# Performance work log

Measured on AMD Instinct MI355X. Metric: run time of the kernel, lower is better.

Reference implementation:

```python
import jax, jax.numpy as jnp
import numpy as np

EPS = 1e-5

def rms_norm(x):
    # SimpleRMSNorm (no learned weight), as used inside BitLinear158
    return x * jax.lax.rsqrt(jnp.mean(x * x, axis=-1, keepdims=True) + EPS)

def act_quant(x):
    # int8 absmax quantization per last-dim row, with straight-through estimator
    scale = 127.0 / jnp.clip(jnp.max(jnp.abs(x), axis=-1, keepdims=True), 1e-5)
    q = jnp.clip(jnp.round(x * scale), -128.0, 127.0) / scale
    return x + jax.lax.stop_gradient(q - x)

def weight_quant(w):
    # ternary {-1,0,1} absmean quantization, with straight-through estimator
    scale = 1.0 / jnp.clip(jnp.mean(jnp.abs(w)), 1e-5)
    q = jnp.clip(jnp.round(w * scale), -1.0, 1.0) / scale
    return w + jax.lax.stop_gradient(q - w)

def bitlinear158(x, w, b):
    xq = act_quant(rms_norm(x))          # [b,s,d_in]
    wq = weight_quant(w)                 # [d_out,d_in]
    return jnp.einsum('bsd,od->bso', xq, wq) + b

def layer_norm(x, g, b):
    mu = jnp.mean(x, axis=-1, keepdims=True)
    var = jnp.mean((x - mu) ** 2, axis=-1, keepdims=True)
    return (x - mu) * jax.lax.rsqrt(var + EPS) * g + b

def setup_inputs() -> dict:
    key = jax.random.key(0)
    ks = jax.random.split(key, 3)
    d, inner = 2048, 8192
    x = jax.random.normal(ks[0], (4, 2048, d), dtype=jnp.float32)
    w1 = jax.random.normal(ks[1], (inner, d), dtype=jnp.float32) * 0.02
    b1 = jnp.zeros((inner,), jnp.float32)
    ln_g = jnp.ones((inner,), jnp.float32)
    ln_b = jnp.zeros((inner,), jnp.float32)
    w2 = jax.random.normal(ks[2], (d, inner), dtype=jnp.float32) * 0.02
    b2 = jnp.zeros((d,), jnp.float32)
    return {"x": x, "w1": w1, "b1": b1, "ln_g": ln_g, "ln_b": ln_b, "w2": w2, "b2": b2}

def reference(x, w1, b1, ln_g, ln_b, w2, b2):
    h = jax.nn.silu(bitlinear158(x, w1, b1))        # project_in: BitLinear158 + SiLU
    h = jax.nn.gelu(h, approximate=False)            # nn.GELU (exact erf form)
    h = layer_norm(h, ln_g, ln_b)                    # nn.LayerNorm(inner_dim)
    return bitlinear158(h, w2, b2)                   # BitLinear158 out projection
```

## Files before the change

### kernel.cpp

```cpp
#include <hip/hip_runtime.h>
#include <hip/hip_bf16.h>
#include <math.h>

typedef __bf16 bf16_t;
typedef __bf16 bf16x4 __attribute__((ext_vector_type(4)));
typedef int i32x4 __attribute__((ext_vector_type(4)));

#define AS1 __attribute__((address_space(1)))
#define AS3 __attribute__((address_space(3)))

__device__ __forceinline__ void gl_lds16(const char* g, char* l) {
  __builtin_amdgcn_global_load_lds((const AS1 void*)g, (AS3 void*)l, 16, 0, 0);
}

__device__ __forceinline__ unsigned pack4i(float a, float b, float c, float d) {
  return ((unsigned)(unsigned char)(int)a) | ((unsigned)(unsigned char)(int)b << 8) |
         ((unsigned)(unsigned char)(int)c << 16) | ((unsigned)(unsigned char)(int)d << 24);
}

__device__ __forceinline__ float block_sum_f(float v) {
  __shared__ float sb[4];
  #pragma unroll
  for (int o = 32; o; o >>= 1) v += __shfl_xor(v, o);
  if ((threadIdx.x & 63) == 0) sb[threadIdx.x >> 6] = v;
  __syncthreads();
  v = sb[0] + sb[1] + sb[2] + sb[3];
  __syncthreads();
  return v;
}
__device__ __forceinline__ float block_max_f(float v) {
  __shared__ float sm[4];
  #pragma unroll
  for (int o = 32; o; o >>= 1) v = fmaxf(v, __shfl_xor(v, o));
  if ((threadIdx.x & 63) == 0) sm[threadIdx.x >> 6] = v;
  __syncthreads();
  v = fmaxf(fmaxf(sm[0], sm[1]), fmaxf(sm[2], sm[3]));
  __syncthreads();
  return v;
}

__global__ __launch_bounds__(256) void wabs_partial(const float* __restrict__ w, int n4,
                                                    double* __restrict__ part) {
  const float4* w4 = (const float4*)w;
  double s = 0.0;
  const int stride = gridDim.x * blockDim.x;
  for (int i = blockIdx.x * blockDim.x + threadIdx.x; i < n4; i += stride) {
    float4 v = w4[i];
    s += (double)fabsf(v.x) + (double)fabsf(v.y) + (double)fabsf(v.z) + (double)fabsf(v.w);
  }
  #pragma unroll
  for (int o = 32; o; o >>= 1) s += __shfl_xor(s, o);
  __shared__ double sd[4];
  if ((threadIdx.x & 63) == 0) sd[threadIdx.x >> 6] = s;
  __syncthreads();
  if (threadIdx.x == 0) part[blockIdx.x] = sd[0] + sd[1] + sd[2] + sd[3];
}

__global__ __launch_bounds__(256) void wabs_final(const double* __restrict__ part, int np,
                                                  double n, float* __restrict__ fwout) {
  double s = 0.0;
  for (int i = threadIdx.x; i < np; i += blockDim.x) s += part[i];
  #pragma unroll
  for (int o = 32; o; o >>= 1) s += __shfl_xor(s, o);
  __shared__ double sd[4];
  if ((threadIdx.x & 63) == 0) sd[threadIdx.x >> 6] = s;
  __syncthreads();
  if (threadIdx.x == 0) {
    double mean = (sd[0] + sd[1] + sd[2] + sd[3]) / n;
    fwout[0] = (float)fmax(mean, 1e-5);
  }
}

__global__ __launch_bounds__(256) void quant_w(const float* __restrict__ w,
                                               const float* __restrict__ fw,
                                               char* __restrict__ wq, int n4) {
  int i = blockIdx.x * blockDim.x + threadIdx.x;
  if (i >= n4) return;
  const float s = 1.0f / fw[0];
  float4 v = ((const float4*)w)[i];
  ((unsigned*)wq)[i] = pack4i(fminf(fmaxf(rintf(v.x * s), -1.f), 1.f),
                              fminf(fmaxf(rintf(v.y * s), -1.f), 1.f),
                              fminf(fmaxf(rintf(v.z * s), -1.f), 1.f),
                              fminf(fmaxf(rintf(v.w * s), -1.f), 1.f));
}

__global__ __launch_bounds__(256) void rms_quant_x(const float* __restrict__ x,
                                                   char* __restrict__ xq,
                                                   float* __restrict__ fx, int K) {
  const int row = blockIdx.x, t = threadIdx.x;
  const size_t base = (size_t)row * K;
  float v[8];
  float ss = 0.f;
  #pragma unroll
  for (int j = 0; j < 2; j++) {
    float4 lv = *(const float4*)(x + base + j * 1024 + t * 4);
    v[j*4+0] = lv.x; v[j*4+1] = lv.y; v[j*4+2] = lv.z; v[j*4+3] = lv.w;
  }
  #pragma unroll
  for (int i = 0; i < 8; i++) ss += v[i] * v[i];
  ss = block_sum_f(ss);
  const float r = 1.0f / sqrtf(ss / (float)K + 1e-5f);
  float amax = 0.f;
  #pragma unroll
  for (int i = 0; i < 8; i++) { v[i] *= r; amax = fmaxf(amax, fabsf(v[i])); }
  amax = block_max_f(amax);
  amax = fmaxf(amax, 1e-5f);
  const float scale = 127.0f / amax;
  #pragma unroll
  for (int j = 0; j < 2; j++) {
    float q[4];
    #pragma unroll
    for (int e = 0; e < 4; e++)
      q[e] = fminf(fmaxf(rintf(v[j*4+e] * scale), -128.f), 127.f);
    *(unsigned*)(xq + base + j * 1024 + t * 4) = pack4i(q[0], q[1], q[2], q[3]);
  }
  if (t == 0) fx[row] = amax / 127.0f;
}

__global__ __launch_bounds__(256) void ln_rms_quant(const bf16_t* __restrict__ h,
                                                    char* __restrict__ hq,
                                                    const float* __restrict__ g,
                                                    const float* __restrict__ bb,
                                                    float* __restrict__ fh, int N) {
  const int row = blockIdx.x, t = threadIdx.x;
  const size_t base = (size_t)row * N;
  float v[32];
  float s = 0.f, ss = 0.f;
  #pragma unroll
  for (int j = 0; j < 8; j++) {
    const int col = j * 1024 + t * 4;
    bf16x4 q = *(const bf16x4*)(h + base + col);
    v[j*4+0] = (float)q[0]; v[j*4+1] = (float)q[1];
    v[j*4+2] = (float)q[2]; v[j*4+3] = (float)q[3];
  }
  #pragma unroll
  for (int i = 0; i < 32; i++) { s += v[i]; ss += v[i] * v[i]; }
  s = block_sum_f(s);
  ss = block_sum_f(ss);
  const float mu = s / (float)N;
  const float var = ss / (float)N - mu * mu;
  const float rstd = 1.0f / sqrtf(var + 1e-5f);
  float ss2 = 0.f;
  #pragma unroll
  for (int j = 0; j < 8; j++) {
    const int col = j * 1024 + t * 4;
    float4 gv = *(const float4*)(g + col);
    float4 bv = *(const float4*)(bb + col);
    float y0 = (v[j*4+0] - mu) * rstd * gv.x + bv.x;
    float y1 = (v[j*4+1] - mu) * rstd * gv.y + bv.y;
    float y2 = (v[j*4+2] - mu) * rstd * gv.z + bv.z;
    float y3 = (v[j*4+3] - mu) * rstd * gv.w + bv.w;
    v[j*4+0] = y0; v[j*4+1] = y1; v[j*4+2] = y2; v[j*4+3] = y3;
    ss2 += y0*y0 + y1*y1 + y2*y2 + y3*y3;
  }
  ss2 = block_sum_f(ss2);
  const float r2 = 1.0f / sqrtf(ss2 / (float)N + 1e-5f);
  float amax = 0.f;
  #pragma unroll
  for (int i = 0; i < 32; i++) { v[i] *= r2; amax = fmaxf(amax, fabsf(v[i])); }
  amax = block_max_f(amax);
  amax = fmaxf(amax, 1e-5f);
  const float scale = 127.0f / amax;
  #pragma unroll
  for (int j = 0; j < 8; j++) {
    const int col = j * 1024 + t * 4;
    float q[4];
    #pragma unroll
    for (int e = 0; e < 4; e++)
      q[e] = fminf(fmaxf(rintf(v[j*4+e] * scale), -128.f), 127.f);
    *(unsigned*)(hq + base + col) = pack4i(q[0], q[1], q[2], q[3]);
  }
  if (t == 0) fh[row] = amax / 127.0f;
}

template<int EPI, bool STORE_BF16>
__global__ __launch_bounds__(512, 2) void gemm256(const char* __restrict__ A,
                                                  const char* __restrict__ B,
                                                  const float* __restrict__ rowf,
                                                  const float* __restrict__ wf,
                                                  const float* __restrict__ bias,
                                                  float* __restrict__ Cf,
                                                  bf16_t* __restrict__ Cb,
                                                  int M, int N, int K) {
  __shared__ char smem[131072];

  const int ntile = N >> 8;
  const int cpx = gridDim.x >> 3;
  const int bid = blockIdx.x;
  const int xcd = bid & 7, local = bid >> 3;
  int wg;
  const int mrows = cpx / ntile;
  if (mrows * ntile == cpx && mrows > 0) {
    const int bm_l = local % mrows, bn_i = local / mrows;
    wg = (xcd * mrows + bm_l) * ntile + bn_i;
  } else {
    wg = xcd * cpx + local;
  }
  const int bm = wg / ntile, bn = wg % ntile;
  const int tm = bm << 8, tn = bn << 8;

  const int tid = threadIdx.x;
  const int w = tid >> 6, lane = tid & 63;
  const int wm = w >> 2, wn = w & 3;
  const int ln15 = lane & 15;

  const int srow = lane >> 3;
  const int scol = ((lane & 7) ^ srow) << 4;
  const size_t KS = (size_t)K;
  const char* pAst = A + (size_t)(tm + w * 16 + srow) * KS + scol;
  const char* pBst = B + (size_t)(tn + w * 16 + srow) * KS + scol;
  const size_t hiO = (size_t)128 * KS;
  const size_t r8 = (size_t)8 * KS;
  const int dW = w * 2048;

  int foffk[2];
  #pragma unroll
  for (int kk = 0; kk < 2; kk++)
    foffk[kk] = ln15 * 128 + ((((kk << 2) + (lane >> 4)) ^ (ln15 & 7)) << 4);

  i32x4 acc[8][4] = {};
  const int NT = K >> 7;

#define SB __builtin_amdgcn_sched_barrier(0)
#define BAR { SB; __builtin_amdgcn_s_barrier(); SB; }
#define ST_A(bb, hh, kt) { const char* p = pAst + ((hh) ? hiO : 0) + (size_t)(kt) * 128; \
    char* dst = smem + (bb) * 32768 + (hh) * 16384 + dW;                                 \
    gl_lds16(p, dst); gl_lds16(p + r8, dst + 1024); }
#define ST_B(bb, hh, kt) { const char* p = pBst + ((hh) ? hiO : 0) + (size_t)(kt) * 128; \
    char* dst = smem + 65536 + (bb) * 32768 + (hh) * 16384 + dW;                         \
    gl_lds16(p, dst); gl_lds16(p + r8, dst + 1024); }
#define MM(AF, BF, MB, NB)                                                   \
  _Pragma("unroll") for (int kk = 0; kk < 2; kk++)                           \
    _Pragma("unroll") for (int m4 = 0; m4 < 4; m4++)                         \
      _Pragma("unroll") for (int n2 = 0; n2 < 2; n2++)                       \
        acc[(MB)+m4][(NB)+n2] = __builtin_amdgcn_mfma_i32_16x16x64_i8(       \
            AF[m4][kk], BF[n2][kk], acc[(MB)+m4][(NB)+n2], 0, 0, 0);
#define VM(n) asm volatile("s_waitcnt vmcnt(" #n ")" ::: "memory")

  ST_A(0, 0, 0); ST_B(0, 0, 0); ST_B(0, 1, 0); ST_A(0, 1, 0);

  for (int t = 0; t < NT; ++t) {
    const int b = t & 1, nb = b ^ 1;
    const char* sA = smem + b * 32768;
    const char* sB = smem + 65536 + b * 32768;
    i32x4 afL[4][2], afH[4][2], bL[2][2], bH[2][2];
    if (t + 1 < NT) { ST_A(nb, 0, t + 1); ST_B(nb, 0, t + 1); VM(8); }
    else            { VM(4); }
    BAR;
    #pragma unroll
    for (int m4 = 0; m4 < 4; m4++)
      #pragma unroll
      for (int kk = 0; kk < 2; kk++)
        afL[m4][kk] = *(const i32x4*)(sA + (wm * 4 + m4) * 2048 + foffk[kk]);
    #pragma unroll
    for (int n2 = 0; n2 < 2; n2++)
      #pragma unroll
      for (int kk = 0; kk < 2; kk++)
        bL[n2][kk] = *(const i32x4*)(sB + (wn * 2 + n2) * 2048 + foffk[kk]);
    __builtin_amdgcn_s_setprio(1);
    MM(afL, bL, 0, 0);
    __builtin_amdgcn_s_setprio(0);
    if (t + 1 < NT) { ST_B(nb, 1, t + 1); VM(8); }
    else            { VM(2); }
    BAR;
    #pragma unroll
    for (int n2 = 0; n2 < 2; n2++)
      #pragma unroll
      for (int kk = 0; kk < 2; kk++)
        bH[n2][kk] = *(const i32x4*)(sB + 16384 + (wn * 2 + n2) * 2048 + foffk[kk]);
    __builtin_amdgcn_s_setprio(1);
    MM(afL, bH, 0, 2);
    __builtin_amdgcn_s_setprio(0);
    if (t + 1 < NT) { ST_A(nb, 1, t + 1); VM(8); }
    else            { VM(0); }
    BAR;
    #pragma unroll
    for (int m4 = 0; m4 < 4; m4++)
      #pragma unroll
      for (int kk = 0; kk < 2; kk++)
        afH[m4][kk] = *(const i32x4*)(sA + 16384 + (wm * 4 + m4) * 2048 + foffk[kk]);
    __builtin_amdgcn_s_setprio(1);
    MM(afH, bH, 4, 2);
    __builtin_amdgcn_s_setprio(0);
    __builtin_amdgcn_s_setprio(1);
    MM(afH, bL, 4, 0);
    __builtin_amdgcn_s_setprio(0);
  }
#undef ST_A
#undef ST_B
#undef MM
#undef VM

  const float fwv = wf[0];
  const int rq = (lane >> 4) << 2;
  float rsc[8][4];
  #pragma unroll
  for (int m = 0; m < 8; m++)
    #pragma unroll
    for (int r = 0; r < 4; r++)
      rsc[m][r] = rowf[tm + (m >> 2) * 128 + wm * 64 + (m & 3) * 16 + rq + r] * fwv;

  #pragma unroll
  for (int m = 0; m < 8; m++) {
    #pragma unroll
    for (int n = 0; n < 4; n++) {
      const int col = tn + (n >> 1) * 128 + wn * 32 + (n & 1) * 16 + ln15;
      const float bv = bias[col];
      #pragma unroll
      for (int r = 0; r < 4; r++) {
        const int row = tm + (m >> 2) * 128 + wm * 64 + (m & 3) * 16 + rq + r;
        float val = (float)acc[m][n][r] * rsc[m][r] + bv;
        if (EPI == 1) {
          float sl = val / (1.0f + __expf(-val));
          val = 0.5f * sl * (1.0f + erff(sl * 0.70710678118654752f));
        }
        if (STORE_BF16) Cb[(size_t)row * N + col] = (bf16_t)val;
        else            Cf[(size_t)row * N + col] = val;
      }
    }
  }
}

extern "C" void kernel_launch(void* const* d_in, const int* in_sizes, int n_in,
                              void* d_out, int out_size, void* d_ws, size_t ws_size,
                              hipStream_t stream) {
  const float* x   = (const float*)d_in[0];
  const float* w1  = (const float*)d_in[1];
  const float* b1  = (const float*)d_in[2];
  const float* lng = (const float*)d_in[3];
  const float* lnb = (const float*)d_in[4];
  const float* w2  = (const float*)d_in[5];
  const float* b2  = (const float*)d_in[6];
  float* out = (float*)d_out;

  const int inner = in_sizes[2];
  const int d     = in_sizes[1] / inner;
  const int M     = in_sizes[0] / d;

  char* ws = (char*)d_ws;
  size_t off = 0;
  double* part = (double*)(ws + off); off += 1024 * 8;
  float*  fw   = (float*)(ws + off);  off += 256;
  float*  fx   = (float*)(ws + off);  off += (size_t)M * 4;
  float*  fh   = (float*)(ws + off);  off += (size_t)M * 4;
  char*   w1q  = ws + off;            off += (size_t)inner * d;
  char*   w2q  = ws + off;            off += (size_t)inner * d;

  int MC = M;
  while (MC > 256 && off + (size_t)MC * ((size_t)d + 3 * (size_t)inner) > ws_size) MC >>= 1;
  char*   xq = ws + off;              off += (size_t)MC * d;
  bf16_t* h  = (bf16_t*)(ws + off);   off += (size_t)MC * inner * 2;
  char*   hq = ws + off;

  const int nw = inner * d;
  const int n4 = nw / 4;

  wabs_partial<<<1024, 256, 0, stream>>>(w1, n4, part);
  wabs_final<<<1, 256, 0, stream>>>(part, 1024, (double)nw, fw + 0);
  wabs_partial<<<1024, 256, 0, stream>>>(w2, n4, part);
  wabs_final<<<1, 256, 0, stream>>>(part, 1024, (double)nw, fw + 1);
  quant_w<<<n4 / 256, 256, 0, stream>>>(w1, fw + 0, w1q, n4);
  quant_w<<<n4 / 256, 256, 0, stream>>>(w2, fw + 1, w2q, n4);

  for (int mc = 0; mc < M; mc += MC) {
    rms_quant_x<<<MC, 256, 0, stream>>>(x + (size_t)mc * d, xq, fx, d);

    const int g1 = (MC / 256) * (inner / 256);
    gemm256<1, true><<<g1, 512, 0, stream>>>(xq, w1q, fx, fw + 0, b1,
                                             nullptr, h, MC, inner, d);

    ln_rms_quant<<<MC, 256, 0, stream>>>(h, hq, lng, lnb, fh, inner);

    const int g2 = (MC / 256) * (d / 256);
    gemm256<0, false><<<g2, 512, 0, stream>>>(hq, w2q, fh, fw + 1, b2,
                                              out + (size_t)mc * d, nullptr, MC, d, inner);
  }
}
```

Baseline: 433.7 us.

## Switch int8 GEMM from 16x16x64 to 32x32x32 MFMA tiles

Replaces the 16x16x64 int8 MFMA instruction with the 32x32x32 variant in the tiled GEMM. Each wave now holds 2x2 32x32 accumulator blocks per half-tile, with LDS fragment offsets and swizzle recomputed for 32-row fragments and the epilogue remapped to the 32x32 output layout. The aim is fewer MFMA issues and fewer LDS fragment reads per unit of work. The trade-offs are a different LDS bank access pattern and higher register pressure from the 16-wide accumulators.

```diff
diff --git a/kernel.cpp b/kernel.cpp
--- a/kernel.cpp
+++ b/kernel.cpp
@@ -5,6 +5,7 @@
 typedef __bf16 bf16_t;
 typedef __bf16 bf16x4 __attribute__((ext_vector_type(4)));
 typedef int i32x4 __attribute__((ext_vector_type(4)));
+typedef int i32x16 __attribute__((ext_vector_type(16)));
 
 #define AS1 __attribute__((address_space(1)))
 #define AS3 __attribute__((address_space(3)))
@@ -202,40 +203,39 @@
   const int tid = threadIdx.x;
   const int w = tid >> 6, lane = tid & 63;
   const int wm = w >> 2, wn = w & 3;
-  const int ln15 = lane & 15;
+  const int ln31 = lane & 31;
 
   const int srow = lane >> 3;
-  const int scol = ((lane & 7) ^ srow) << 4;
+  const int scol = ((lane & 7) ^ (lane >> 3)) << 4;
   const size_t KS = (size_t)K;
   const char* pAst = A + (size_t)(tm + w * 16 + srow) * KS + scol;
   const char* pBst = B + (size_t)(tn + w * 16 + srow) * KS + scol;
   const size_t hiO = (size_t)128 * KS;
-  const size_t r8 = (size_t)8 * KS;
+  const size_t r8v = (size_t)8 * KS;
   const int dW = w * 2048;
 
-  int foffk[2];
-  #pragma unroll
-  for (int kk = 0; kk < 2; kk++)
-    foffk[kk] = ln15 * 128 + ((((kk << 2) + (lane >> 4)) ^ (ln15 & 7)) << 4);
-
-  i32x4 acc[8][4] = {};
+  int foffk[4];
+  #pragma unroll
+  for (int kk = 0; kk < 4; kk++)
+    foffk[kk] = ln31 * 128 + ((((kk << 1) + (lane >> 5)) ^ (lane & 7)) << 4);
+
+  i32x16 acc[4][2] = {};
   const int NT = K >> 7;
 
 #define SB __builtin_amdgcn_sched_barrier(0)
 #define BAR { SB; __builtin_amdgcn_s_barrier(); SB; }
+#define VM(n) asm volatile("s_waitcnt vmcnt(" #n ")" ::: "memory")
 #define ST_A(bb, hh, kt) { const char* p = pAst + ((hh) ? hiO : 0) + (size_t)(kt) * 128; \
     char* dst = smem + (bb) * 32768 + (hh) * 16384 + dW;                                 \
-    gl_lds16(p, dst); gl_lds16(p + r8, dst + 1024); }
+    gl_lds16(p, dst); gl_lds16(p + r8v, dst + 1024); }
 #define ST_B(bb, hh, kt) { const char* p = pBst + ((hh) ? hiO : 0) + (size_t)(kt) * 128; \
     char* dst = smem + 65536 + (bb) * 32768 + (hh) * 16384 + dW;                         \
-    gl_lds16(p, dst); gl_lds16(p + r8, dst + 1024); }
-#define MM(AF, BF, MB, NB)                                                   \
-  _Pragma("unroll") for (int kk = 0; kk < 2; kk++)                           \
-    _Pragma("unroll") for (int m4 = 0; m4 < 4; m4++)                         \
-      _Pragma("unroll") for (int n2 = 0; n2 < 2; n2++)                       \
-        acc[(MB)+m4][(NB)+n2] = __builtin_amdgcn_mfma_i32_16x16x64_i8(       \
-            AF[m4][kk], BF[n2][kk], acc[(MB)+m4][(NB)+n2], 0, 0, 0);
-#define VM(n) asm volatile("s_waitcnt vmcnt(" #n ")" ::: "memory")
+    gl_lds16(p, dst); gl_lds16(p + r8v, dst + 1024); }
+#define MMQ(AF, BF, MB, NB)                                                  \
+  _Pragma("unroll") for (int mfl = 0; mfl < 2; mfl++)                        \
+    _Pragma("unroll") for (int kk = 0; kk < 4; kk++)                         \
+      acc[(MB)+mfl][NB] = __builtin_amdgcn_mfma_i32_32x32x32_i8(             \
+          AF[mfl][kk], BF[kk], acc[(MB)+mfl][NB], 0, 0, 0);
 
   ST_A(0, 0, 0); ST_B(0, 0, 0); ST_B(0, 1, 0); ST_A(0, 1, 0);
 
@@ -243,79 +243,76 @@
     const int b = t & 1, nb = b ^ 1;
     const char* sA = smem + b * 32768;
     const char* sB = smem + 65536 + b * 32768;
-    i32x4 afL[4][2], afH[4][2], bL[2][2], bH[2][2];
+    i32x4 afL[2][4], afH[2][4], bL[4], bH[4];
     if (t + 1 < NT) { ST_A(nb, 0, t + 1); ST_B(nb, 0, t + 1); VM(8); }
     else            { VM(4); }
     BAR;
     #pragma unroll
-    for (int m4 = 0; m4 < 4; m4++)
+    for (int mfl = 0; mfl < 2; mfl++)
       #pragma unroll
-      for (int kk = 0; kk < 2; kk++)
-        afL[m4][kk] = *(const i32x4*)(sA + (wm * 4 + m4) * 2048 + foffk[kk]);
-    #pragma unroll
-    for (int n2 = 0; n2 < 2; n2++)
-      #pragma unroll
-      for (int kk = 0; kk < 2; kk++)
-        bL[n2][kk] = *(const i32x4*)(sB + (wn * 2 + n2) * 2048 + foffk[kk]);
+      for (int kk = 0; kk < 4; kk++)
+        afL[mfl][kk] = *(const i32x4*)(sA + (wm * 2 + mfl) * 4096 + foffk[kk]);
+    #pragma unroll
+    for (int kk = 0; kk < 4; kk++)
+      bL[kk] = *(const i32x4*)(sB + wn * 4096 + foffk[kk]);
     __builtin_amdgcn_s_setprio(1);
-    MM(afL, bL, 0, 0);
+    MMQ(afL, bL, 0, 0);
     __builtin_amdgcn_s_setprio(0);
     if (t + 1 < NT) { ST_B(nb, 1, t + 1); VM(8); }
     else            { VM(2); }
     BAR;
     #pragma unroll
-    for (int n2 = 0; n2 < 2; n2++)
-      #pragma unroll
-      for (int kk = 0; kk < 2; kk++)
-        bH[n2][kk] = *(const i32x4*)(sB + 16384 + (wn * 2 + n2) * 2048 + foffk[kk]);
+    for (int kk = 0; kk < 4; kk++)
+      bH[kk] = *(const i32x4*)(sB + 16384 + wn * 4096 + foffk[kk]);
     __builtin_amdgcn_s_setprio(1);
-    MM(afL, bH, 0, 2);
+    MMQ(afL, bH, 0, 1);
     __builtin_amdgcn_s_setprio(0);
     if (t + 1 < NT) { ST_A(nb, 1, t + 1); VM(8); }
     else            { VM(0); }
     BAR;
     #pragma unroll
-    for (int m4 = 0; m4 < 4; m4++)
+    for (int mfl = 0; mfl < 2; mfl++)
       #pragma unroll
-      for (int kk = 0; kk < 2; kk++)
-        afH[m4][kk] = *(const i32x4*)(sA + 16384 + (wm * 4 + m4) * 2048 + foffk[kk]);
+      for (int kk = 0; kk < 4; kk++)
+        afH[mfl][kk] = *(const i32x4*)(sA + 16384 + (wm * 2 + mfl) * 4096 + foffk[kk]);
     __builtin_amdgcn_s_setprio(1);
-    MM(afH, bH, 4, 2);
+    MMQ(afH, bH, 2, 1);
     __builtin_amdgcn_s_setprio(0);
     __builtin_amdgcn_s_setprio(1);
-    MM(afH, bL, 4, 0);
+    MMQ(afH, bL, 2, 0);
     __builtin_amdgcn_s_setprio(0);
   }
 #undef ST_A
 #undef ST_B
-#undef MM
+#undef MMQ
 #undef VM
 
   const float fwv = wf[0];
-  const int rq = (lane >> 4) << 2;
-  float rsc[8][4];
-  #pragma unroll
-  for (int m = 0; m < 8; m++)
-    #pragma unroll
-    for (int r = 0; r < 4; r++)
-      rsc[m][r] = rowf[tm + (m >> 2) * 128 + wm * 64 + (m & 3) * 16 + rq + r] * fwv;
-
-  #pragma unroll
-  for (int m = 0; m < 8; m++) {
-    #pragma unroll
-    for (int n = 0; n < 4; n++) {
-      const int col = tn + (n >> 1) * 128 + wn * 32 + (n & 1) * 16 + ln15;
-      const float bv = bias[col];
+  const int rbase = (lane >> 5) << 2;
+  #pragma unroll
+  for (int mh = 0; mh < 2; mh++) {
+    #pragma unroll
+    for (int mfl = 0; mfl < 2; mfl++) {
+      const int rowb = tm + mh * 128 + wm * 64 + mfl * 32;
+      float rsc[16];
       #pragma unroll
-      for (int r = 0; r < 4; r++) {
-        const int row = tm + (m >> 2) * 128 + wm * 64 + (m & 3) * 16 + rq + r;
-        float val = (float)acc[m][n][r] * rsc[m][r] + bv;
-        if (EPI == 1) {
-          float sl = val / (1.0f + __expf(-val));
-          val = 0.5f * sl * (1.0f + erff(sl * 0.70710678118654752f));
+      for (int g = 0; g < 16; g++)
+        rsc[g] = rowf[rowb + (g & 3) + 8 * (g >> 2) + rbase] * fwv;
+      #pragma unroll
+      for (int nh = 0; nh < 2; nh++) {
+        const int col = tn + nh * 128 + wn * 32 + ln31;
+        const float bv = bias[col];
+        #pragma unroll
+        for (int g = 0; g < 16; g++) {
+          const int row = rowb + (g & 3) + 8 * (g >> 2) + rbase;
+          float val = (float)acc[mh * 2 + mfl][nh][g] * rsc[g] + bv;
+          if (EPI == 1) {
+            float sl = val / (1.0f + __expf(-val));
+            val = 0.5f * sl * (1.0f + erff(sl * 0.70710678118654752f));
+          }
+          if (STORE_BF16) Cb[(size_t)row * N + col] = (bf16_t)val;
+          else            Cf[(size_t)row * N + col] = val;
         }
-        if (STORE_BF16) Cb[(size_t)row * N + col] = (bf16_t)val;
-        else            Cf[(size_t)row * N + col] = val;
       }
     }
   }
```

After: 463.4 us. 1.07x slower.
